# Kernel tuning notes

Hardware: AMD Instinct MI355X
Metric: run time of the kernel (lower is better)

The kernel has to match this reference:

```python
import jax, jax.numpy as jnp
import numpy as np
import math

B, S, D, H, L, F = 32, 512, 512, 8, 4, 2048
DK = D // H
EPS = 1e-5


def _cosine_pos_emb(seq_len, d_model):
    pe = np.zeros((seq_len, d_model), dtype=np.float32)
    position = np.arange(seq_len, dtype=np.float32)[:, None]
    div_term = np.exp(np.arange(0, d_model, 2, dtype=np.float32) * (-math.log(10000.0) / d_model))
    pe[:, 0::2] = np.sin(position * div_term)
    pe[:, 1::2] = np.cos(position * div_term)
    return jnp.asarray(pe[None])  # (1, S, D)


def setup_inputs() -> dict:
    key = jax.random.key(0)
    ks = jax.random.split(key, 12)
    w = 0.02
    return {
        "q_embed_data": jax.random.normal(ks[0], (B, S, D), jnp.float32),
        "qa_embed_data": jax.random.normal(ks[1], (B, S, D), jnp.float32),
        "forget_rate": jax.random.uniform(ks[2], (B, S, 1), jnp.float32),
        "pos_emb": _cosine_pos_emb(S, D),
        # per-layer stacked params (torch Linear convention: W is (out,in))
        "Wk": w * jax.random.normal(ks[3], (L, D, D), jnp.float32),
        "bk": jnp.zeros((L, D), jnp.float32),
        "Wv": w * jax.random.normal(ks[4], (L, D, D), jnp.float32),
        "bv": jnp.zeros((L, D), jnp.float32),
        "Wo": w * jax.random.normal(ks[5], (L, D, D), jnp.float32),
        "bo": jnp.zeros((L, D), jnp.float32),
        "W1": w * jax.random.normal(ks[6], (L, F, D), jnp.float32),
        "b1": jnp.zeros((L, F), jnp.float32),
        "W2": w * jax.random.normal(ks[7], (L, D, F), jnp.float32),
        "b2": jnp.zeros((L, D), jnp.float32),
        "ln1_g": jnp.ones((L, D), jnp.float32),
        "ln1_b": jnp.zeros((L, D), jnp.float32),
        "ln2_g": jnp.ones((L, D), jnp.float32),
        "ln2_b": jnp.zeros((L, D), jnp.float32),
    }


def _layer_norm(x, g, b):
    mu = jnp.mean(x, axis=-1, keepdims=True)
    var = jnp.mean(jnp.square(x - mu), axis=-1, keepdims=True)
    return (x - mu) * jax.lax.rsqrt(var + EPS) * g + b


def _forward(q_embed_data, qa_embed_data, forget_rate, pos_emb,
             Wk, bk, Wv, bv, Wo, bo, W1, b1, W2, b2,
             ln1_g, ln1_b, ln2_g, ln2_b):
    x = q_embed_data + pos_emb   # queries/keys stream
    y = qa_embed_data + pos_emb  # values stream (fixed across layers)
    scale = 1.0 / math.sqrt(DK)
    # mask=0 path: triu(k=0)==0 -> strictly past positions only (j < i)
    allowed = jnp.tril(jnp.ones((S, S), dtype=bool), k=-1)
    fr = forget_rate[:, None, :, :]  # (B,1,S,1): row-wise decay on scores
    neg = jnp.asarray(-1e32, x.dtype)

    def block(x, p):
        wk, bk_, wv, bv_, wo, bo_, w1, b1_, w2, b2_, g1, be1, g2, be2 = p
        # kq_same=1: q and k share the k_linear projection (so q == k here)
        kq = (jnp.einsum('bsd,ed->bse', x, wk) + bk_).reshape(B, S, H, DK).transpose(0, 2, 1, 3)
        v = (jnp.einsum('bsd,ed->bse', y, wv) + bv_).reshape(B, S, H, DK).transpose(0, 2, 1, 3)
        scores = jnp.einsum('bhsd,bhtd->bhst', kq, kq) * scale
        scores = scores * fr
        scores = jnp.where(allowed, scores, neg)
        attn = jax.nn.softmax(scores, axis=-1)
        attn = attn.at[:, :, 0, :].set(0.0)  # zero_pad: first query row zeroed
        ctx = jnp.einsum('bhst,bhtd->bhsd', attn, v).transpose(0, 2, 1, 3).reshape(B, S, D)
        out = jnp.einsum('bsd,ed->bse', ctx, wo) + bo_
        x = _layer_norm(x + out, g1, be1)
        ff = jnp.einsum('bsf,df->bsd', jax.nn.relu(jnp.einsum('bsd,fd->bsf', x, w1) + b1_), w2) + b2_
        x = _layer_norm(x + ff, g2, be2)
        return x, None

    x, _ = jax.lax.scan(block, x, (Wk, bk, Wv, bv, Wo, bo, W1, b1, W2, b2, ln1_g, ln1_b, ln2_g, ln2_b))
    return x


def reference(q_embed_data, qa_embed_data, forget_rate, pos_emb,
              Wk, bk, Wv, bv, Wo, bo, W1, b1, W2, b2,
              ln1_g, ln1_b, ln2_g, ln2_b):
    return _forward(q_embed_data, qa_embed_data, forget_rate, pos_emb,
                    Wk, bk, Wv, bv, Wo, bo, W1, b1, W2, b2,
                    ln1_g, ln1_b, ln2_g, ln2_b)
```

## Files before the change

### kernel.cpp

```cpp
#include <hip/hip_runtime.h>
#include <hip/hip_bf16.h>

constexpr int B_ = 32, S_ = 512, D_ = 512, H_ = 8, L_ = 4, F_ = 2048, DK_ = 64;

typedef __attribute__((ext_vector_type(8))) short short8;
typedef __attribute__((ext_vector_type(4))) float f32x4;
typedef __attribute__((ext_vector_type(16))) float f32x16;

__device__ inline unsigned short f2b(float f) {
  union { __hip_bfloat16 h; unsigned short u; } cv;
  cv.h = __float2bfloat16(f);
  return cv.u;
}
__device__ inline float b2f(unsigned short u) {
  union { unsigned int i; float f; } c;
  c.i = ((unsigned int)u) << 16;
  return c.f;
}
__device__ inline unsigned pkbf(float a, float b) {
  unsigned r;
  asm("v_cvt_pk_bf16_f32 %0, %1, %2" : "=v"(r) : "v"(a), "v"(b));
  return r;
}
__device__ inline float waveReduceSum(float v) {
  #pragma unroll
  for (int o = 32; o > 0; o >>= 1) v += __shfl_xor(v, o);
  return v;
}

__global__ void prep_kernel(const float4* __restrict__ q, const float4* __restrict__ qa,
                            const float4* __restrict__ pos, float4* __restrict__ xf,
                            uint2* __restrict__ xb, uint2* __restrict__ yb) {
  int i = blockIdx.x * blockDim.x + threadIdx.x;
  float4 p = pos[i & 65535];
  float4 a = q[i], c = qa[i];
  float4 xv, yv;
  xv.x = a.x + p.x; xv.y = a.y + p.y; xv.z = a.z + p.z; xv.w = a.w + p.w;
  yv.x = c.x + p.x; yv.y = c.y + p.y; yv.z = c.z + p.z; yv.w = c.w + p.w;
  xf[i] = xv;
  uint2 px, py;
  px.x = (unsigned)f2b(xv.x) | ((unsigned)f2b(xv.y) << 16);
  px.y = (unsigned)f2b(xv.z) | ((unsigned)f2b(xv.w) << 16);
  py.x = (unsigned)f2b(yv.x) | ((unsigned)f2b(yv.y) << 16);
  py.y = (unsigned)f2b(yv.z) | ((unsigned)f2b(yv.w) << 16);
  xb[i] = px;
  yb[i] = py;
}

__global__ void cast_kernel(const float4* __restrict__ src, uint2* __restrict__ dst, int n4) {
  int i = blockIdx.x * blockDim.x + threadIdx.x;
  if (i >= n4) return;
  float4 v = src[i];
  uint2 p;
  p.x = (unsigned)f2b(v.x) | ((unsigned)f2b(v.y) << 16);
  p.y = (unsigned)f2b(v.z) | ((unsigned)f2b(v.w) << 16);
  dst[i] = p;
}

template<int RELU, int STORE>
__global__ __launch_bounds__(256, 2) void gemm128_kernel(
    const __hip_bfloat16* __restrict__ A,
    const __hip_bfloat16* __restrict__ W,
    const float* __restrict__ bias,
    const __hip_bfloat16* __restrict__ A2,
    const __hip_bfloat16* __restrict__ W2,
    const float* __restrict__ bias2,
    __hip_bfloat16* __restrict__ Cb,
    __hip_bfloat16* __restrict__ Cb2,
    int Ndim, int Kdim, int kLen)
{
  __shared__ char lds[32768];
  const int tid = threadIdx.x, wave = tid >> 6, lane = tid & 63;
  const int rl = lane & 15, gq = lane >> 4;
  const int wr = wave >> 1, wc = wave & 1;

  const int nwg = gridDim.x * gridDim.y;
  const int lin = blockIdx.y * gridDim.x + blockIdx.x;
  const int swz = (lin & 7) * (nwg >> 3) + (lin >> 3);
  const int bx = swz % gridDim.x, by = swz / gridDim.x;

  const int row0 = by * 128;
  const int col0 = bx * 128;

  const __hip_bfloat16* Ap = A;
  const __hip_bfloat16* Wp = W;
  const float* bp = bias;
  int kOff = blockIdx.z * kLen;
  if (STORE == 3) {
    kOff = 0;
    if (blockIdx.z) { Ap = A2; Wp = W2; bp = bias2; }
  }

  f32x4 acc[4][4] = {};
  const int ntiles = kLen >> 5;

  auto stage = [&](int kt, int d) {
    const int kbase = kOff + (kt << 5);
    #pragma unroll
    for (int r = 0; r < 2; ++r) {
      int p = r * 4096 + tid * 16;
      int R = p >> 6, c = (p >> 4) & 3;
      int gc = c ^ ((R >> 1) & 3);
      const __hip_bfloat16* srcA = Ap + (size_t)(row0 + R) * Kdim + kbase + gc * 8;
      __builtin_amdgcn_global_load_lds(
          (const __attribute__((address_space(1))) void*)srcA,
          (__attribute__((address_space(3))) void*)(lds + d * 8192 + p), 16, 0, 0);
      const __hip_bfloat16* srcW = Wp + (size_t)(col0 + R) * Kdim + kbase + gc * 8;
      __builtin_amdgcn_global_load_lds(
          (const __attribute__((address_space(1))) void*)srcW,
          (__attribute__((address_space(3))) void*)(lds + 16384 + d * 8192 + p), 16, 0, 0);
    }
  };

  stage(0, 0);
  __syncthreads();
  for (int kt = 0; kt < ntiles; ++kt) {
    const int d = kt & 1;
    if (kt + 1 < ntiles) stage(kt + 1, d ^ 1);

    short8 aF[4], bF[4];
    #pragma unroll
    for (int m = 0; m < 4; ++m) {
      int rr = wr * 64 + m * 16 + rl;
      aF[m] = *(const short8*)(lds + d * 8192 + rr * 64 + ((gq ^ ((rr >> 1) & 3)) << 4));
    }
    #pragma unroll
    for (int n = 0; n < 4; ++n) {
      int rr = wc * 64 + n * 16 + rl;
      bF[n] = *(const short8*)(lds + 16384 + d * 8192 + rr * 64 + ((gq ^ ((rr >> 1) & 3)) << 4));
    }
    __builtin_amdgcn_s_setprio(1);
    #pragma unroll
    for (int m = 0; m < 4; ++m)
      #pragma unroll
      for (int n = 0; n < 4; ++n)
        acc[m][n] = __builtin_amdgcn_mfma_f32_16x16x32_bf16(aF[m], bF[n], acc[m][n], 0, 0, 0);
    __builtin_amdgcn_s_setprio(0);
    __syncthreads();
  }

  char* sw = lds + wave * 8192;
  const bool vt = (STORE == 3) && (blockIdx.z == 1);
  const bool addb = (STORE == 3) ? true : ((bias != nullptr) && (blockIdx.z == 0));
  float bvv[4];
  #pragma unroll
  for (int n = 0; n < 4; ++n)
    bvv[n] = addb ? bp[col0 + wc * 64 + n * 16 + rl] : 0.0f;

  #pragma unroll
  for (int n = 0; n < 4; ++n)
    #pragma unroll
    for (int m = 0; m < 4; ++m)
      #pragma unroll
      for (int j = 0; j < 4; ++j) {
        float val = acc[m][n][j] + bvv[n];
        if (RELU) val = fmaxf(val, 0.0f);
        int addr;
        if (vt) {
          int orow = n * 16 + rl, ocol = m * 16 + gq * 4 + j;
          addr = orow * 128 + ((ocol * 2) ^ ((orow & 7) << 4));
        } else {
          int orow = m * 16 + gq * 4 + j;
          addr = orow * 128 + (((n * 16 + rl) * 2) ^ (((orow >> 1) & 7) << 4));
        }
        *(unsigned short*)(sw + addr) = f2b(val);
      }
  asm volatile("s_waitcnt lgkmcnt(0)" ::: "memory");
  __builtin_amdgcn_sched_barrier(0);

  __hip_bfloat16* Cbd = blockIdx.z ? Cb2 : Cb;
  const int cchunk = lane & 7;
  if (vt) {
    const int bh64 = ((row0 >> 9) * 8 + (col0 >> 6) + wc) * 64;
    const int tbase = (row0 & 511) + wr * 64;
    #pragma unroll
    for (int it = 0; it < 8; ++it) {
      int d0 = it * 8 + (lane >> 3);
      uint4 vv = *(const uint4*)(sw + d0 * 128 + ((cchunk * 16) ^ ((d0 & 7) << 4)));
      *(uint4*)((char*)Cbd + ((size_t)(bh64 + d0) * 512 + tbase) * 2 + cchunk * 16) = vv;
    }
  } else {
    #pragma unroll
    for (int it = 0; it < 8; ++it) {
      int orow = it * 8 + (lane >> 3);
      uint4 vv = *(const uint4*)(sw + orow * 128 + ((cchunk * 16) ^ (((orow >> 1) & 7) << 4)));
      *(uint4*)((char*)Cbd + ((size_t)(row0 + wr * 64 + orow) * Ndim + col0 + wc * 64) * 2 +
                cchunk * 16) = vv;
    }
  }
}

__global__ __launch_bounds__(512, 2) void fattn_kernel(
    const __hip_bfloat16* __restrict__ kq,
    const __hip_bfloat16* __restrict__ vT,
    const float* __restrict__ fr,
    __hip_bfloat16* __restrict__ ctx)
{
  __shared__ char lds[131072];
  const int tid = threadIdx.x, wave = tid >> 6, lane = tid & 63;
  const int lq = lane & 31, hi = lane >> 5;
  const int bh = blockIdx.x;
  const int b = bh >> 3, h = bh & 7;
  const size_t kqbase = ((size_t)b * S_) * D_ + h * DK_;
  const size_t vtbase = ((size_t)bh * DK_) * S_;
  const char* kg = (const char*)kq + kqbase * 2;
  const char* vg = (const char*)vT + vtbase * 2;

  #pragma unroll
  for (int i = 0; i < 8; ++i) {
    int p = i * 8192 + tid * 16;
    int r = p >> 7, ck = (p >> 4) & 7;
    __builtin_amdgcn_global_load_lds(
        (const __attribute__((address_space(1))) void*)(kg + (size_t)r * 1024 + ((ck ^ (r & 7)) << 4)),
        (__attribute__((address_space(3))) void*)(lds + p), 16, 0, 0);
  }
  #pragma unroll
  for (int i = 0; i < 8; ++i) {
    int p = i * 8192 + tid * 16;
    int d = p >> 10, ck = (p >> 4) & 63;
    __builtin_amdgcn_global_load_lds(
        (const __attribute__((address_space(1))) void*)(vg + (size_t)d * 1024 + ((ck ^ (d & 15)) << 4)),
        (__attribute__((address_space(3))) void*)(lds + 65536 + p), 16, 0, 0);
  }

  const int qia = wave, qib = 15 - wave;
  const int na = qia + 1, nb = qib + 1;
  const int sa = qia * 32 + lq, sb = qib * 32 + lq;
  const float sfa = fr[b * S_ + sa] * 0.125f;
  const float sfb = fr[b * S_ + sb] * 0.125f;

  asm volatile("s_waitcnt vmcnt(0)" ::: "memory");
  __builtin_amdgcn_sched_barrier(0);
  __builtin_amdgcn_s_barrier();

  short8 qa_[4], qb_[4];
  #pragma unroll
  for (int f = 0; f < 4; ++f) {
    qa_[f] = *(const short8*)(lds + sa * 128 + ((((f << 1) + hi) ^ (sa & 7)) << 4));
    qb_[f] = *(const short8*)(lds + sb * 128 + ((((f << 1) + hi) ^ (sb & 7)) << 4));
  }

  f32x16 oa0 = {}, oa1 = {}, ob0 = {}, ob1 = {};
  float ma = -3.0e38f, la = 0.0f, mb = -3.0e38f, lb = 0.0f;

  auto process = [&](f32x16& o0, f32x16& o1, float& m, float& l,
                     const short8* qf, int srow, float sf,
                     const short8* kb, const short8* vb0, const short8* vb1,
                     int t0) {
    f32x16 s = {};
    #pragma unroll
    for (int f = 0; f < 4; ++f)
      s = __builtin_amdgcn_mfma_f32_32x32x16_bf16(kb[f], qf[f], s, 0, 0, 0);
    float p[16];
    #pragma unroll
    for (int r = 0; r < 16; ++r) {
      int tg = t0 + (r & 3) + 8 * (r >> 2) + 4 * hi;
      float v = s[r] * sf;
      p[r] = (tg >= srow) ? -3.0e38f : v;
    }
    float t8[8], t4[4];
    #pragma unroll
    for (int i = 0; i < 8; ++i) t8[i] = fmaxf(p[2 * i], p[2 * i + 1]);
    #pragma unroll
    for (int i = 0; i < 4; ++i) t4[i] = fmaxf(t8[2 * i], t8[2 * i + 1]);
    float mt = fmaxf(fmaxf(t4[0], t4[1]), fmaxf(t4[2], t4[3]));
    mt = fmaxf(mt, __shfl_xor(mt, 32));
    float mn = fmaxf(m, mt);
    float fac = __expf(m - mn);
    m = mn;
    l *= fac;
    #pragma unroll
    for (int r = 0; r < 16; ++r) p[r] = __expf(p[r] - mn);
    float s8[8], s4[4];
    #pragma unroll
    for (int i = 0; i < 8; ++i) s8[i] = p[2 * i] + p[2 * i + 1];
    #pragma unroll
    for (int i = 0; i < 4; ++i) s4[i] = s8[2 * i] + s8[2 * i + 1];
    float ps = (s4[0] + s4[1]) + (s4[2] + s4[3]);
    ps += __shfl_xor(ps, 32);
    l += ps;
    #pragma unroll
    for (int i = 0; i < 16; ++i) { o0[i] *= fac; o1[i] *= fac; }
    #pragma unroll
    for (int c = 0; c < 2; ++c) {
      unsigned X0 = pkbf(p[8 * c + 0], p[8 * c + 1]);
      unsigned X1 = pkbf(p[8 * c + 2], p[8 * c + 3]);
      unsigned Y0 = pkbf(p[8 * c + 4], p[8 * c + 5]);
      unsigned Y1 = pkbf(p[8 * c + 6], p[8 * c + 7]);
      unsigned z0 = hi ? X0 : Y0, z1 = hi ? X1 : Y1;
      unsigned r0 = __shfl_xor(z0, 32), r1 = __shfl_xor(z1, 32);
      union { unsigned u[4]; short8 v; } pb;
      pb.u[0] = hi ? r0 : X0;
      pb.u[1] = hi ? r1 : X1;
      pb.u[2] = hi ? Y0 : r0;
      pb.u[3] = hi ? Y1 : r1;
      o0 = __builtin_amdgcn_mfma_f32_32x32x16_bf16(vb0[c], pb.v, o0, 0, 0, 0);
      o1 = __builtin_amdgcn_mfma_f32_32x32x16_bf16(vb1[c], pb.v, o1, 0, 0, 0);
    }
  };

  for (int ti = 0; ti < nb; ++ti) {
    const int t0 = ti * 32;
    short8 kb[4];
    #pragma unroll
    for (int f = 0; f < 4; ++f) {
      int tw = t0 + lq;
      kb[f] = *(const short8*)(lds + tw * 128 + ((((f << 1) + hi) ^ (tw & 7)) << 4));
    }
    short8 vb0[2], vb1[2];
    #pragma unroll
    for (int c = 0; c < 2; ++c) {
      int ck = 4 * ti + 2 * c + hi;
      int d0 = lq;
      vb0[c] = *(const short8*)(lds + 65536 + d0 * 1024 + ((ck ^ (d0 & 15)) << 4));
      int d1 = 32 + lq;
      vb1[c] = *(const short8*)(lds + 65536 + d1 * 1024 + ((ck ^ (d1 & 15)) << 4));
    }
    if (ti < na) process(oa0, oa1, ma, la, qa_, sa, sfa, kb, vb0, vb1, t0);
    process(ob0, ob1, mb, lb, qb_, sb, sfb, kb, vb0, vb1, t0);
  }

  auto writeO = [&](const f32x16& o0, const f32x16& o1, float l, int srow) {
    float inv = (srow == 0) ? 0.0f : 1.0f / l;
    char* base = (char*)ctx + (((size_t)(b * S_ + srow)) * D_ + h * DK_) * 2;
    #pragma unroll
    for (int g = 0; g < 4; ++g) {
      uint2 w0, w1;
      w0.x = pkbf(o0[4 * g + 0] * inv, o0[4 * g + 1] * inv);
      w0.y = pkbf(o0[4 * g + 2] * inv, o0[4 * g + 3] * inv);
      *(uint2*)(base + (8 * g + 4 * hi) * 2) = w0;
      w1.x = pkbf(o1[4 * g + 0] * inv, o1[4 * g + 1] * inv);
      w1.y = pkbf(o1[4 * g + 2] * inv, o1[4 * g + 3] * inv);
      *(uint2*)(base + (32 + 8 * g + 4 * hi) * 2) = w1;
    }
  };
  writeO(oa0, oa1, la, sa);
  writeO(ob0, ob1, lb, sb);
}

template<int NADD>
__global__ __launch_bounds__(256) void ln_kernel(
    const float4* __restrict__ xin, const uint4* __restrict__ add,
    const uint4* __restrict__ add2,
    const float* __restrict__ g, const float* __restrict__ bta,
    float4* xf_out, uint2* __restrict__ xb_out)
{
  const int lane = threadIdx.x & 63, wv = threadIdx.x >> 6;
  const size_t row = (size_t)blockIdx.x * 4 + wv;
  const size_t base4 = row * 128;

  float4 x0 = xin[base4 + lane * 2], x1 = xin[base4 + lane * 2 + 1];
  uint4 ab = add[row * 64 + lane];
  const unsigned short* ap = (const unsigned short*)&ab;
  float v[8];
  v[0] = x0.x; v[1] = x0.y; v[2] = x0.z; v[3] = x0.w;
  v[4] = x1.x; v[5] = x1.y; v[6] = x1.z; v[7] = x1.w;
  #pragma unroll
  for (int i = 0; i < 8; ++i) v[i] += b2f(ap[i]);
  if (NADD == 2) {
    uint4 ab2 = add2[row * 64 + lane];
    const unsigned short* ap2 = (const unsigned short*)&ab2;
    #pragma unroll
    for (int i = 0; i < 8; ++i) v[i] += b2f(ap2[i]);
  }
  float s = 0.0f;
  #pragma unroll
  for (int i = 0; i < 8; ++i) s += v[i];
  s = waveReduceSum(s);
  float mu = s * (1.0f / 512.0f);
  float vs = 0.0f;
  #pragma unroll
  for (int i = 0; i < 8; ++i) { float dd = v[i] - mu; vs += dd * dd; }
  vs = waveReduceSum(vs);
  float rstd = rsqrtf(vs * (1.0f / 512.0f) + 1e-5f);

  const int c0i = lane * 8;
  float4 gg0 = *(const float4*)(g + c0i), gg1 = *(const float4*)(g + c0i + 4);
  float4 bb0 = *(const float4*)(bta + c0i), bb1 = *(const float4*)(bta + c0i + 4);
  float o[8];
  o[0] = (v[0] - mu) * rstd * gg0.x + bb0.x;
  o[1] = (v[1] - mu) * rstd * gg0.y + bb0.y;
  o[2] = (v[2] - mu) * rstd * gg0.z + bb0.z;
  o[3] = (v[3] - mu) * rstd * gg0.w + bb0.w;
  o[4] = (v[4] - mu) * rstd * gg1.x + bb1.x;
  o[5] = (v[5] - mu) * rstd * gg1.y + bb1.y;
  o[6] = (v[6] - mu) * rstd * gg1.z + bb1.z;
  o[7] = (v[7] - mu) * rstd * gg1.w + bb1.w;
  float4 w0, w1;
  w0.x = o[0]; w0.y = o[1]; w0.z = o[2]; w0.w = o[3];
  w1.x = o[4]; w1.y = o[5]; w1.z = o[6]; w1.w = o[7];
  xf_out[base4 + lane * 2] = w0;
  xf_out[base4 + lane * 2 + 1] = w1;
  uint2 p0, p1;
  p0.x = (unsigned)f2b(o[0]) | ((unsigned)f2b(o[1]) << 16);
  p0.y = (unsigned)f2b(o[2]) | ((unsigned)f2b(o[3]) << 16);
  p1.x = (unsigned)f2b(o[4]) | ((unsigned)f2b(o[5]) << 16);
  p1.y = (unsigned)f2b(o[6]) | ((unsigned)f2b(o[7]) << 16);
  xb_out[row * 128 + lane * 2] = p0;
  xb_out[row * 128 + lane * 2 + 1] = p1;
}

extern "C" void kernel_launch(void* const* d_in, const int* in_sizes, int n_in,
                              void* d_out, int out_size, void* d_ws, size_t ws_size,
                              hipStream_t stream) {
  (void)in_sizes; (void)n_in; (void)out_size; (void)ws_size;
  const float* q   = (const float*)d_in[0];
  const float* qa  = (const float*)d_in[1];
  const float* frr = (const float*)d_in[2];
  const float* pos = (const float*)d_in[3];
  const float* Wk  = (const float*)d_in[4];
  const float* bk  = (const float*)d_in[5];
  const float* Wv  = (const float*)d_in[6];
  const float* bv  = (const float*)d_in[7];
  const float* Wo  = (const float*)d_in[8];
  const float* bo  = (const float*)d_in[9];
  const float* W1  = (const float*)d_in[10];
  const float* b1  = (const float*)d_in[11];
  const float* W2  = (const float*)d_in[12];
  const float* b2  = (const float*)d_in[13];
  const float* g1  = (const float*)d_in[14];
  const float* be1 = (const float*)d_in[15];
  const float* g2  = (const float*)d_in[16];
  const float* be2 = (const float*)d_in[17];

  char* ws = (char*)d_ws;
  float*          xf   = (float*)(ws + 0);
  __hip_bfloat16* xb   = (__hip_bfloat16*)(ws + 33554432);
  __hip_bfloat16* yb   = (__hip_bfloat16*)(ws + 50331648);
  __hip_bfloat16* kqb  = (__hip_bfloat16*)(ws + 67108864);
  __hip_bfloat16* vtb  = (__hip_bfloat16*)(ws + 83886080);
  __hip_bfloat16* ctxb = (__hip_bfloat16*)(ws + 100663296);
  __hip_bfloat16* hb   = (__hip_bfloat16*)(ws + 117440512);
  __hip_bfloat16* wkb  = (__hip_bfloat16*)(ws + 184549376);
  __hip_bfloat16* wvb  = (__hip_bfloat16*)(ws + 186646528);
  __hip_bfloat16* wob  = (__hip_bfloat16*)(ws + 188743680);
  __hip_bfloat16* w1b  = (__hip_bfloat16*)(ws + 190840832);
  __hip_bfloat16* w2b  = (__hip_bfloat16*)(ws + 199229440);
  __hip_bfloat16* obf = (__hip_bfloat16*)(ws + 67108864);
  __hip_bfloat16* pf0 = (__hip_bfloat16*)(ws + 83886080);
  __hip_bfloat16* pf1 = (__hip_bfloat16*)(ws + 100663296);

  prep_kernel<<<8192, 256, 0, stream>>>((const float4*)q, (const float4*)qa,
                                        (const float4*)pos, (float4*)xf,
                                        (uint2*)xb, (uint2*)yb);
  cast_kernel<<<1024, 256, 0, stream>>>((const float4*)Wk, (uint2*)wkb, 262144);
  cast_kernel<<<1024, 256, 0, stream>>>((const float4*)Wv, (uint2*)wvb, 262144);
  cast_kernel<<<1024, 256, 0, stream>>>((const float4*)Wo, (uint2*)wob, 262144);
  cast_kernel<<<4096, 256, 0, stream>>>((const float4*)W1, (uint2*)w1b, 1048576);
  cast_kernel<<<4096, 256, 0, stream>>>((const float4*)W2, (uint2*)w2b, 1048576);

  for (int l = 0; l < L_; ++l) {
    gemm128_kernel<0,3><<<dim3(4, 128, 2), 256, 0, stream>>>(
        xb, wkb + (size_t)l * 262144, bk + l * 512,
        yb, wvb + (size_t)l * 262144, bv + l * 512,
        kqb, vtb, 512, 512, 512);
    fattn_kernel<<<256, 512, 0, stream>>>(kqb, vtb, frr, ctxb);
    gemm128_kernel<0,0><<<dim3(4, 128, 1), 256, 0, stream>>>(
        ctxb, wob + (size_t)l * 262144, bo + l * 512,
        nullptr, nullptr, nullptr, obf, nullptr, 512, 512, 512);
    ln_kernel<1><<<4096, 256, 0, stream>>>((const float4*)xf, (const uint4*)obf, nullptr,
                                           g1 + l * 512, be1 + l * 512,
                                           (float4*)xf, (uint2*)xb);
    gemm128_kernel<1,0><<<dim3(16, 128, 1), 256, 0, stream>>>(
        xb, w1b + (size_t)l * 1048576, b1 + l * 2048,
        nullptr, nullptr, nullptr, hb, nullptr, 2048, 512, 512);
    gemm128_kernel<0,0><<<dim3(4, 128, 2), 256, 0, stream>>>(
        hb, w2b + (size_t)l * 1048576, b2 + l * 512,
        nullptr, nullptr, nullptr, pf0, pf1, 512, 2048, 1024);
    float* lnout = (l == L_ - 1) ? (float*)d_out : xf;
    ln_kernel<2><<<4096, 256, 0, stream>>>((const float4*)xf, (const uint4*)pf0,
                                           (const uint4*)pf1,
                                           g2 + l * 512, be2 + l * 512,
                                           (float4*)lnout, (uint2*)xb);
  }
}
```

Before: 793.2 us.

## Fuse output-projection and FFN2 GEMMs with residual add and LayerNorm

```diff
diff --git a/kernel.cpp b/kernel.cpp
--- a/kernel.cpp
+++ b/kernel.cpp
@@ -21,11 +21,6 @@
   unsigned r;
   asm("v_cvt_pk_bf16_f32 %0, %1, %2" : "=v"(r) : "v"(a), "v"(b));
   return r;
-}
-__device__ inline float waveReduceSum(float v) {
-  #pragma unroll
-  for (int o = 32; o > 0; o >>= 1) v += __shfl_xor(v, o);
-  return v;
 }
 
 __global__ void prep_kernel(const float4* __restrict__ q, const float4* __restrict__ qa,
@@ -190,6 +185,134 @@
   }
 }
 
+__global__ __launch_bounds__(256, 2) void gemmln_kernel(
+    const __hip_bfloat16* __restrict__ A,
+    const __hip_bfloat16* __restrict__ W,
+    const float* __restrict__ bias,
+    const float* __restrict__ xres,
+    const float* __restrict__ g, const float* __restrict__ beta,
+    float* __restrict__ xf_out,
+    unsigned short* __restrict__ xb_out,
+    int Kdim)
+{
+  __shared__ char lds[70656];
+  const int tid = threadIdx.x, wave = tid >> 6, lane = tid & 63;
+  const int rl = lane & 15, gq = lane >> 4;
+
+  const int swz = (blockIdx.x & 7) * (gridDim.x >> 3) + (blockIdx.x >> 3);
+  const int row0 = swz * 32;
+
+  f32x4 acc[2][8] = {};
+  const int ntiles = Kdim >> 5;
+
+  auto stage = [&](int kt, int d) {
+    const int kbase = kt << 5;
+    if (tid < 128) {
+      int p = tid * 16;
+      int R = p >> 6, c = (p >> 4) & 3;
+      int gc = c ^ ((R >> 1) & 3);
+      const __hip_bfloat16* srcA = A + (size_t)(row0 + R) * Kdim + kbase + gc * 8;
+      __builtin_amdgcn_global_load_lds(
+          (const __attribute__((address_space(1))) void*)srcA,
+          (__attribute__((address_space(3))) void*)(lds + d * 2048 + p), 16, 0, 0);
+    }
+    #pragma unroll
+    for (int r = 0; r < 8; ++r) {
+      int p = r * 4096 + tid * 16;
+      int R = p >> 6, c = (p >> 4) & 3;
+      int gc = c ^ ((R >> 1) & 3);
+      const __hip_bfloat16* srcW = W + (size_t)R * Kdim + kbase + gc * 8;
+      __builtin_amdgcn_global_load_lds(
+          (const __attribute__((address_space(1))) void*)srcW,
+          (__attribute__((address_space(3))) void*)(lds + 4096 + d * 32768 + p), 16, 0, 0);
+    }
+  };
+
+  stage(0, 0);
+  __syncthreads();
+  for (int kt = 0; kt < ntiles; ++kt) {
+    const int d = kt & 1;
+    if (kt + 1 < ntiles) stage(kt + 1, d ^ 1);
+
+    short8 aF[2], bF[8];
+    #pragma unroll
+    for (int m = 0; m < 2; ++m) {
+      int rr = m * 16 + rl;
+      aF[m] = *(const short8*)(lds + d * 2048 + rr * 64 + ((gq ^ ((rr >> 1) & 3)) << 4));
+    }
+    #pragma unroll
+    for (int n = 0; n < 8; ++n) {
+      int rr = wave * 128 + n * 16 + rl;
+      bF[n] = *(const short8*)(lds + 4096 + d * 32768 + rr * 64 + ((gq ^ ((rr >> 1) & 3)) << 4));
+    }
+    __builtin_amdgcn_s_setprio(1);
+    #pragma unroll
+    for (int m = 0; m < 2; ++m)
+      #pragma unroll
+      for (int n = 0; n < 8; ++n)
+        acc[m][n] = __builtin_amdgcn_mfma_f32_16x16x32_bf16(aF[m], bF[n], acc[m][n], 0, 0, 0);
+    __builtin_amdgcn_s_setprio(0);
+    __syncthreads();
+  }
+
+  float* red = (float*)(lds + 69632);
+  float bvn[8], gvn[8], btn[8];
+  #pragma unroll
+  for (int n = 0; n < 8; ++n) {
+    int col = wave * 128 + n * 16 + rl;
+    bvn[n] = bias[col];
+    gvn[n] = g[col];
+    btn[n] = beta[col];
+  }
+
+  #pragma unroll
+  for (int m = 0; m < 2; ++m)
+    #pragma unroll
+    for (int j = 0; j < 4; ++j) {
+      int rowloc = m * 16 + gq * 4 + j;
+      size_t rb = (size_t)(row0 + rowloc) * 512 + wave * 128 + rl;
+      float s = 0.0f, qq = 0.0f;
+      #pragma unroll
+      for (int n = 0; n < 8; ++n) {
+        float v = acc[m][n][j] + bvn[n] + xres[rb + n * 16];
+        acc[m][n][j] = v;
+        s += v;
+        qq += v * v;
+      }
+      #pragma unroll
+      for (int msk = 1; msk < 16; msk <<= 1) {
+        s += __shfl_xor(s, msk);
+        qq += __shfl_xor(qq, msk);
+      }
+      if (rl == 0) {
+        red[rowloc * 8 + wave * 2 + 0] = s;
+        red[rowloc * 8 + wave * 2 + 1] = qq;
+      }
+    }
+  __syncthreads();
+
+  #pragma unroll
+  for (int m = 0; m < 2; ++m)
+    #pragma unroll
+    for (int j = 0; j < 4; ++j) {
+      int rowloc = m * 16 + gq * 4 + j;
+      float s = red[rowloc * 8 + 0] + red[rowloc * 8 + 2] +
+                red[rowloc * 8 + 4] + red[rowloc * 8 + 6];
+      float qq = red[rowloc * 8 + 1] + red[rowloc * 8 + 3] +
+                 red[rowloc * 8 + 5] + red[rowloc * 8 + 7];
+      float mu = s * (1.0f / 512.0f);
+      float var = qq * (1.0f / 512.0f) - mu * mu;
+      float rstd = rsqrtf(var + 1e-5f);
+      size_t rb = (size_t)(row0 + rowloc) * 512 + wave * 128 + rl;
+      #pragma unroll
+      for (int n = 0; n < 8; ++n) {
+        float o = (acc[m][n][j] - mu) * rstd * gvn[n] + btn[n];
+        xf_out[rb + n * 16] = o;
+        xb_out[rb + n * 16] = f2b(o);
+      }
+    }
+}
+
 __global__ __launch_bounds__(512, 2) void fattn_kernel(
     const __hip_bfloat16* __restrict__ kq,
     const __hip_bfloat16* __restrict__ vT,
@@ -324,80 +447,18 @@
     float inv = (srow == 0) ? 0.0f : 1.0f / l;
     char* base = (char*)ctx + (((size_t)(b * S_ + srow)) * D_ + h * DK_) * 2;
     #pragma unroll
-    for (int g = 0; g < 4; ++g) {
+    for (int gg = 0; gg < 4; ++gg) {
       uint2 w0, w1;
-      w0.x = pkbf(o0[4 * g + 0] * inv, o0[4 * g + 1] * inv);
-      w0.y = pkbf(o0[4 * g + 2] * inv, o0[4 * g + 3] * inv);
-      *(uint2*)(base + (8 * g + 4 * hi) * 2) = w0;
-      w1.x = pkbf(o1[4 * g + 0] * inv, o1[4 * g + 1] * inv);
-      w1.y = pkbf(o1[4 * g + 2] * inv, o1[4 * g + 3] * inv);
-      *(uint2*)(base + (32 + 8 * g + 4 * hi) * 2) = w1;
+      w0.x = pkbf(o0[4 * gg + 0] * inv, o0[4 * gg + 1] * inv);
+      w0.y = pkbf(o0[4 * gg + 2] * inv, o0[4 * gg + 3] * inv);
+      *(uint2*)(base + (8 * gg + 4 * hi) * 2) = w0;
+      w1.x = pkbf(o1[4 * gg + 0] * inv, o1[4 * gg + 1] * inv);
+      w1.y = pkbf(o1[4 * gg + 2] * inv, o1[4 * gg + 3] * inv);
+      *(uint2*)(base + (32 + 8 * gg + 4 * hi) * 2) = w1;
     }
   };
   writeO(oa0, oa1, la, sa);
   writeO(ob0, ob1, lb, sb);
-}
-
-template<int NADD>
-__global__ __launch_bounds__(256) void ln_kernel(
-    const float4* __restrict__ xin, const uint4* __restrict__ add,
-    const uint4* __restrict__ add2,
-    const float* __restrict__ g, const float* __restrict__ bta,
-    float4* xf_out, uint2* __restrict__ xb_out)
-{
-  const int lane = threadIdx.x & 63, wv = threadIdx.x >> 6;
-  const size_t row = (size_t)blockIdx.x * 4 + wv;
-  const size_t base4 = row * 128;
-
-  float4 x0 = xin[base4 + lane * 2], x1 = xin[base4 + lane * 2 + 1];
-  uint4 ab = add[row * 64 + lane];
-  const unsigned short* ap = (const unsigned short*)&ab;
-  float v[8];
-  v[0] = x0.x; v[1] = x0.y; v[2] = x0.z; v[3] = x0.w;
-  v[4] = x1.x; v[5] = x1.y; v[6] = x1.z; v[7] = x1.w;
-  #pragma unroll
-  for (int i = 0; i < 8; ++i) v[i] += b2f(ap[i]);
-  if (NADD == 2) {
-    uint4 ab2 = add2[row * 64 + lane];
-    const unsigned short* ap2 = (const unsigned short*)&ab2;
-    #pragma unroll
-    for (int i = 0; i < 8; ++i) v[i] += b2f(ap2[i]);
-  }
-  float s = 0.0f;
-  #pragma unroll
-  for (int i = 0; i < 8; ++i) s += v[i];
-  s = waveReduceSum(s);
-  float mu = s * (1.0f / 512.0f);
-  float vs = 0.0f;
-  #pragma unroll
-  for (int i = 0; i < 8; ++i) { float dd = v[i] - mu; vs += dd * dd; }
-  vs = waveReduceSum(vs);
-  float rstd = rsqrtf(vs * (1.0f / 512.0f) + 1e-5f);
-
-  const int c0i = lane * 8;
-  float4 gg0 = *(const float4*)(g + c0i), gg1 = *(const float4*)(g + c0i + 4);
-  float4 bb0 = *(const float4*)(bta + c0i), bb1 = *(const float4*)(bta + c0i + 4);
-  float o[8];
-  o[0] = (v[0] - mu) * rstd * gg0.x + bb0.x;
-  o[1] = (v[1] - mu) * rstd * gg0.y + bb0.y;
-  o[2] = (v[2] - mu) * rstd * gg0.z + bb0.z;
-  o[3] = (v[3] - mu) * rstd * gg0.w + bb0.w;
-  o[4] = (v[4] - mu) * rstd * gg1.x + bb1.x;
-  o[5] = (v[5] - mu) * rstd * gg1.y + bb1.y;
-  o[6] = (v[6] - mu) * rstd * gg1.z + bb1.z;
-  o[7] = (v[7] - mu) * rstd * gg1.w + bb1.w;
-  float4 w0, w1;
-  w0.x = o[0]; w0.y = o[1]; w0.z = o[2]; w0.w = o[3];
-  w1.x = o[4]; w1.y = o[5]; w1.z = o[6]; w1.w = o[7];
-  xf_out[base4 + lane * 2] = w0;
-  xf_out[base4 + lane * 2 + 1] = w1;
-  uint2 p0, p1;
-  p0.x = (unsigned)f2b(o[0]) | ((unsigned)f2b(o[1]) << 16);
-  p0.y = (unsigned)f2b(o[2]) | ((unsigned)f2b(o[3]) << 16);
-  p1.x = (unsigned)f2b(o[4]) | ((unsigned)f2b(o[5]) << 16);
-  p1.y = (unsigned)f2b(o[6]) | ((unsigned)f2b(o[7]) << 16);
-  xb_out[row * 128 + lane * 2] = p0;
-  xb_out[row * 128 + lane * 2 + 1] = p1;
 }
 
 extern "C" void kernel_launch(void* const* d_in, const int* in_sizes, int n_in,
@@ -436,9 +497,6 @@
   __hip_bfloat16* wob  = (__hip_bfloat16*)(ws + 188743680);
   __hip_bfloat16* w1b  = (__hip_bfloat16*)(ws + 190840832);
   __hip_bfloat16* w2b  = (__hip_bfloat16*)(ws + 199229440);
-  __hip_bfloat16* obf = (__hip_bfloat16*)(ws + 67108864);
-  __hip_bfloat16* pf0 = (__hip_bfloat16*)(ws + 83886080);
-  __hip_bfloat16* pf1 = (__hip_bfloat16*)(ws + 100663296);
 
   prep_kernel<<<8192, 256, 0, stream>>>((const float4*)q, (const float4*)qa,
                                         (const float4*)pos, (float4*)xf,
@@ -455,22 +513,17 @@
         yb, wvb + (size_t)l * 262144, bv + l * 512,
         kqb, vtb, 512, 512, 512);
     fattn_kernel<<<256, 512, 0, stream>>>(kqb, vtb, frr, ctxb);
-    gemm128_kernel<0,0><<<dim3(4, 128, 1), 256, 0, stream>>>(
+    gemmln_kernel<<<512, 256, 0, stream>>>(
         ctxb, wob + (size_t)l * 262144, bo + l * 512,
-        nullptr, nullptr, nullptr, obf, nullptr, 512, 512, 512);
-    ln_kernel<1><<<4096, 256, 0, stream>>>((const float4*)xf, (const uint4*)obf, nullptr,
-                                           g1 + l * 512, be1 + l * 512,
-                                           (float4*)xf, (uint2*)xb);
+        xf, g1 + l * 512, be1 + l * 512,
+        xf, (unsigned short*)xb, 512);
     gemm128_kernel<1,0><<<dim3(16, 128, 1), 256, 0, stream>>>(
         xb, w1b + (size_t)l * 1048576, b1 + l * 2048,
         nullptr, nullptr, nullptr, hb, nullptr, 2048, 512, 512);
-    gemm128_kernel<0,0><<<dim3(4, 128, 2), 256, 0, stream>>>(
+    float* lnout = (l == L_ - 1) ? (float*)d_out : xf;
+    gemmln_kernel<<<512, 256, 0, stream>>>(
         hb, w2b + (size_t)l * 1048576, b2 + l * 512,
-        nullptr, nullptr, nullptr, pf0, pf1, 512, 2048, 1024);
-    float* lnout = (l == L_ - 1) ? (float*)d_out : xf;
-    ln_kernel<2><<<4096, 256, 0, stream>>>((const float4*)xf, (const uint4*)pf0,
-                                           (const uint4*)pf1,
-                                           g2 + l * 512, be2 + l * 512,
-                                           (float4*)lnout, (uint2*)xb);
-  }
-}
+        xf, g2 + l * 512, be2 + l * 512,
+        lnout, (unsigned short*)xb, 2048);
+  }
+}
```

Result: slower. 880.0 us (+10.9%).

## Use 256x256-tile 8-wave GEMM with 4-stage LDS pipeline for FFN1

Applied to the files above, without the earlier changes.

```diff
diff --git a/kernel.cpp b/kernel.cpp
--- a/kernel.cpp
+++ b/kernel.cpp
@@ -190,6 +190,173 @@
   }
 }
 
+template<int RELU>
+__global__ __launch_bounds__(512, 2) void gemm256_8p_kernel(
+    const __hip_bfloat16* __restrict__ A,
+    const __hip_bfloat16* __restrict__ W,
+    const float* __restrict__ bias,
+    __hip_bfloat16* __restrict__ Cb,
+    int Ndim, int Kdim)
+{
+  __shared__ char lds[131072];
+  const int tid = threadIdx.x, wave = tid >> 6, lane = tid & 63;
+  const int rl = lane & 15, gq = lane >> 4;
+  const int wr = wave >> 2, wc = wave & 3;
+
+  const int nwg = gridDim.x * gridDim.y;
+  const int lin = blockIdx.y * gridDim.x + blockIdx.x;
+  const int swz = (lin & 7) * (nwg >> 3) + (lin >> 3);
+  const int bx = swz % gridDim.x, by = swz / gridDim.x;
+  const int row0 = by * 256;
+  const int col0 = bx * 256;
+
+  f32x4 acc[8][4] = {};
+  const int ntiles = Kdim >> 5;
+
+  auto stage = [&](int kt) {
+    const int buf = kt & 3;
+    const int kbase = kt << 5;
+    #pragma unroll
+    for (int r = 0; r < 2; ++r) {
+      int p = r * 8192 + tid * 16;
+      int R = p >> 6, c = (p >> 4) & 3;
+      int gc = c ^ ((R >> 1) & 3);
+      const __hip_bfloat16* srcA = A + (size_t)(row0 + R) * Kdim + kbase + gc * 8;
+      __builtin_amdgcn_global_load_lds(
+          (const __attribute__((address_space(1))) void*)srcA,
+          (__attribute__((address_space(3))) void*)(lds + buf * 16384 + p), 16, 0, 0);
+    }
+    #pragma unroll
+    for (int r = 0; r < 2; ++r) {
+      int p = r * 8192 + tid * 16;
+      int R = p >> 6, c = (p >> 4) & 3;
+      int gc = c ^ ((R >> 1) & 3);
+      const __hip_bfloat16* srcW = W + (size_t)(col0 + R) * Kdim + kbase + gc * 8;
+      __builtin_amdgcn_global_load_lds(
+          (const __attribute__((address_space(1))) void*)srcW,
+          (__attribute__((address_space(3))) void*)(lds + 65536 + buf * 16384 + p), 16, 0, 0);
+    }
+  };
+
+  stage(0); stage(1); stage(2);
+  asm volatile("s_waitcnt vmcnt(8)" ::: "memory");
+  __builtin_amdgcn_sched_barrier(0);
+  __builtin_amdgcn_s_barrier();
+  __builtin_amdgcn_sched_barrier(0);
+
+  for (int kt = 0; kt < ntiles; ++kt) {
+    const int abase = (kt & 3) * 16384;
+    const int wbase = 65536 + (kt & 3) * 16384;
+
+    short8 bF[4], aF[4];
+    #pragma unroll
+    for (int n = 0; n < 4; ++n) {
+      int rr = wc * 64 + n * 16 + rl;
+      bF[n] = *(const short8*)(lds + wbase + rr * 64 + ((gq ^ ((rr >> 1) & 3)) << 4));
+    }
+    #pragma unroll
+    for (int m = 0; m < 4; ++m) {
+      int rr = wr * 128 + m * 16 + rl;
+      aF[m] = *(const short8*)(lds + abase + rr * 64 + ((gq ^ ((rr >> 1) & 3)) << 4));
+    }
+    if (kt + 3 < ntiles) {
+      const int buf = (kt + 3) & 3;
+      const int kbase = (kt + 3) << 5;
+      #pragma unroll
+      for (int r = 0; r < 2; ++r) {
+        int p = r * 8192 + tid * 16;
+        int R = p >> 6, c = (p >> 4) & 3;
+        int gc = c ^ ((R >> 1) & 3);
+        const __hip_bfloat16* srcA = A + (size_t)(row0 + R) * Kdim + kbase + gc * 8;
+        __builtin_amdgcn_global_load_lds(
+            (const __attribute__((address_space(1))) void*)srcA,
+            (__attribute__((address_space(3))) void*)(lds + buf * 16384 + p), 16, 0, 0);
+      }
+    }
+    asm volatile("s_waitcnt lgkmcnt(0)" ::: "memory");
+    __builtin_amdgcn_sched_barrier(0);
+    __builtin_amdgcn_s_setprio(1);
+    #pragma unroll
+    for (int m = 0; m < 4; ++m)
+      #pragma unroll
+      for (int n = 0; n < 4; ++n)
+        acc[m][n] = __builtin_amdgcn_mfma_f32_16x16x32_bf16(aF[m], bF[n], acc[m][n], 0, 0, 0);
+    __builtin_amdgcn_s_setprio(0);
+
+    short8 aG[4];
+    #pragma unroll
+    for (int m = 0; m < 4; ++m) {
+      int rr = wr * 128 + 64 + m * 16 + rl;
+      aG[m] = *(const short8*)(lds + abase + rr * 64 + ((gq ^ ((rr >> 1) & 3)) << 4));
+    }
+    if (kt + 3 < ntiles) {
+      const int buf = (kt + 3) & 3;
+      const int kbase = (kt + 3) << 5;
+      #pragma unroll
+      for (int r = 0; r < 2; ++r) {
+        int p = r * 8192 + tid * 16;
+        int R = p >> 6, c = (p >> 4) & 3;
+        int gc = c ^ ((R >> 1) & 3);
+        const __hip_bfloat16* srcW = W + (size_t)(col0 + R) * Kdim + kbase + gc * 8;
+        __builtin_amdgcn_global_load_lds(
+            (const __attribute__((address_space(1))) void*)srcW,
+            (__attribute__((address_space(3))) void*)(lds + 65536 + buf * 16384 + p), 16, 0, 0);
+      }
+    }
+    asm volatile("s_waitcnt lgkmcnt(0)" ::: "memory");
+    __builtin_amdgcn_sched_barrier(0);
+    __builtin_amdgcn_s_setprio(1);
+    #pragma unroll
+    for (int m = 0; m < 4; ++m)
+      #pragma unroll
+      for (int n = 0; n < 4; ++n)
+        acc[4 + m][n] = __builtin_amdgcn_mfma_f32_16x16x32_bf16(aG[m], bF[n], acc[4 + m][n], 0, 0, 0);
+    __builtin_amdgcn_s_setprio(0);
+
+    if (kt + 3 < ntiles) {
+      asm volatile("s_waitcnt vmcnt(8)" ::: "memory");
+    } else if (kt + 2 < ntiles) {
+      asm volatile("s_waitcnt vmcnt(4)" ::: "memory");
+    } else {
+      asm volatile("s_waitcnt vmcnt(0)" ::: "memory");
+    }
+    __builtin_amdgcn_sched_barrier(0);
+    __builtin_amdgcn_s_barrier();
+    __builtin_amdgcn_sched_barrier(0);
+  }
+
+  __syncthreads();
+  char* sw = lds + wave * 16384;
+  float bvv[4];
+  #pragma unroll
+  for (int n = 0; n < 4; ++n)
+    bvv[n] = bias[col0 + wc * 64 + n * 16 + rl];
+
+  #pragma unroll
+  for (int mm = 0; mm < 8; ++mm)
+    #pragma unroll
+    for (int n = 0; n < 4; ++n)
+      #pragma unroll
+      for (int j = 0; j < 4; ++j) {
+        float val = acc[mm][n][j] + bvv[n];
+        if (RELU) val = fmaxf(val, 0.0f);
+        int orow = (mm >> 2) * 64 + (mm & 3) * 16 + gq * 4 + j;
+        int addr = orow * 128 + (((n * 16 + rl) * 2) ^ (((orow >> 1) & 7) << 4));
+        *(unsigned short*)(sw + addr) = f2b(val);
+      }
+  asm volatile("s_waitcnt lgkmcnt(0)" ::: "memory");
+  __builtin_amdgcn_sched_barrier(0);
+
+  const int cchunk = lane & 7;
+  #pragma unroll
+  for (int it = 0; it < 16; ++it) {
+    int orow = it * 8 + (lane >> 3);
+    uint4 vv = *(const uint4*)(sw + orow * 128 + ((cchunk * 16) ^ (((orow >> 1) & 7) << 4)));
+    *(uint4*)((char*)Cb + ((size_t)(row0 + wr * 128 + orow) * Ndim + col0 + wc * 64) * 2 +
+              cchunk * 16) = vv;
+  }
+}
+
 __global__ __launch_bounds__(512, 2) void fattn_kernel(
     const __hip_bfloat16* __restrict__ kq,
     const __hip_bfloat16* __restrict__ vT,
@@ -324,14 +491,14 @@
     float inv = (srow == 0) ? 0.0f : 1.0f / l;
     char* base = (char*)ctx + (((size_t)(b * S_ + srow)) * D_ + h * DK_) * 2;
     #pragma unroll
-    for (int g = 0; g < 4; ++g) {
+    for (int gg = 0; gg < 4; ++gg) {
       uint2 w0, w1;
-      w0.x = pkbf(o0[4 * g + 0] * inv, o0[4 * g + 1] * inv);
-      w0.y = pkbf(o0[4 * g + 2] * inv, o0[4 * g + 3] * inv);
-      *(uint2*)(base + (8 * g + 4 * hi) * 2) = w0;
-      w1.x = pkbf(o1[4 * g + 0] * inv, o1[4 * g + 1] * inv);
-      w1.y = pkbf(o1[4 * g + 2] * inv, o1[4 * g + 3] * inv);
-      *(uint2*)(base + (32 + 8 * g + 4 * hi) * 2) = w1;
+      w0.x = pkbf(o0[4 * gg + 0] * inv, o0[4 * gg + 1] * inv);
+      w0.y = pkbf(o0[4 * gg + 2] * inv, o0[4 * gg + 3] * inv);
+      *(uint2*)(base + (8 * gg + 4 * hi) * 2) = w0;
+      w1.x = pkbf(o1[4 * gg + 0] * inv, o1[4 * gg + 1] * inv);
+      w1.y = pkbf(o1[4 * gg + 2] * inv, o1[4 * gg + 3] * inv);
+      *(uint2*)(base + (32 + 8 * gg + 4 * hi) * 2) = w1;
     }
   };
   writeO(oa0, oa1, la, sa);
@@ -461,9 +628,8 @@
     ln_kernel<1><<<4096, 256, 0, stream>>>((const float4*)xf, (const uint4*)obf, nullptr,
                                            g1 + l * 512, be1 + l * 512,
                                            (float4*)xf, (uint2*)xb);
-    gemm128_kernel<1,0><<<dim3(16, 128, 1), 256, 0, stream>>>(
-        xb, w1b + (size_t)l * 1048576, b1 + l * 2048,
-        nullptr, nullptr, nullptr, hb, nullptr, 2048, 512, 512);
+    gemm256_8p_kernel<1><<<dim3(8, 64), 512, 0, stream>>>(
+        xb, w1b + (size_t)l * 1048576, b1 + l * 2048, hb, 2048, 512);
     gemm128_kernel<0,0><<<dim3(4, 128, 2), 256, 0, stream>>>(
         hb, w2b + (size_t)l * 1048576, b2 + l * 512,
         nullptr, nullptr, nullptr, pf0, pf1, 512, 2048, 1024);
```

Result: no change. 787.9 us (-0.7%).
